# Performance work log

Measured on AMD Instinct MI355X. Metric: run time of the kernel, lower is better.

The kernel has to match this reference:

```python
import jax, jax.numpy as jnp
import numpy as np
from jax import lax

GAT_SLOPE = 0.2   # leaky relu slope inside GATv2 attention
MLP_SLOPE = 0.01  # default nn.LeakyReLU slope in the MLP


def setup_inputs() -> dict:
    key = jax.random.key(0)
    ks = iter(jax.random.split(key, 48))
    nm, nd, C, H = 1500, 800, 128, 8
    E, P = 80000, 40000

    def nrm(shape, s=0.1):
        return jax.random.normal(next(ks), shape, jnp.float32) * s

    inp = {
        "mic_feature": nrm((nm, nm), 1.0),
        "dis_feature": nrm((nd, nd), 1.0),
        "edge_index": jax.random.randint(next(ks), (2, E), 0, nm + nd),
        "pos_pairs": jnp.stack([jax.random.randint(next(ks), (P,), 0, nm),
                                 jax.random.randint(next(ks), (P,), 0, nd)], axis=1),
        "neg_pairs": jnp.stack([jax.random.randint(next(ks), (P,), 0, nm),
                                 jax.random.randint(next(ks), (P,), 0, nd)], axis=1),
        "train_model": 1,
        # projection params
        "W_mic": nrm((nm, C)),
        "W_dis": nrm((nd, C)),
        # GATv2Conv params (lin_l, lin_r, att, out bias); concat=True -> out dim H*C
        "gat_Wl": nrm((C, H * C)),
        "gat_bl": jnp.zeros((H * C,), jnp.float32),
        "gat_Wr": nrm((C, H * C)),
        "gat_br": jnp.zeros((H * C,), jnp.float32),
        "gat_att": nrm((H, C)),
        "gat_bias": jnp.zeros((H * C,), jnp.float32),
        # CNN kernels (heads, k) for k in {1,4,16,32}, 6 out channels
        "cw1": nrm((6, 1, H, 1)),  "cb1": jnp.zeros((6,), jnp.float32),
        "cw4": nrm((6, 1, H, 4)),  "cb4": jnp.zeros((6,), jnp.float32),
        "cw16": nrm((6, 1, H, 16)), "cb16": jnp.zeros((6,), jnp.float32),
        "cw32": nrm((6, 1, H, 32)), "cb32": jnp.zeros((6,), jnp.float32),
        # MLP: 2778 -> 1389 -> 694 -> 463 -> 1 (no bias on last)
        "mw1": nrm((2778, 1389), 0.02), "mb1": jnp.zeros((1389,), jnp.float32),
        "mw2": nrm((1389, 694), 0.02),  "mb2": jnp.zeros((694,), jnp.float32),
        "mw3": nrm((694, 463), 0.02),   "mb3": jnp.zeros((463,), jnp.float32),
        "mw4": nrm((463, 1), 0.05),
    }
    return inp


def _lrelu(x, s):
    return jnp.where(x > 0, x, s * x)


def reference(mic_feature, dis_feature, edge_index, pos_pairs, neg_pairs, train_model,
              W_mic, W_dis, gat_Wl, gat_bl, gat_Wr, gat_br, gat_att, gat_bias,
              cw1, cb1, cw4, cb4, cw16, cb16, cw32, cb32,
              mw1, mb1, mw2, mb2, mw3, mb3, mw4):
    H = gat_att.shape[0]
    # project both node types to common dim and stack: [N, C]
    h = jnp.concatenate([mic_feature @ W_mic, dis_feature @ W_dis], axis=0)
    N, C = h.shape
    # GATv2: separate source/target transforms -> [N, H, C]
    xl = (h @ gat_Wl + gat_bl).reshape(N, H, C)
    xr = (h @ gat_Wr + gat_br).reshape(N, H, C)
    # add self loops (PyG default)
    src = jnp.concatenate([edge_index[0], jnp.arange(N)])
    dst = jnp.concatenate([edge_index[1], jnp.arange(N)])
    z = _lrelu(xl[src] + xr[dst], GAT_SLOPE)           # [E, H, C]
    e = jnp.einsum('ehc,hc->eh', z, gat_att)           # [E, H]
    # segment softmax over incoming edges per destination node
    emax = jax.ops.segment_max(e, dst, num_segments=N)
    ex = jnp.exp(e - emax[dst])
    den = jax.ops.segment_sum(ex, dst, num_segments=N)
    alpha = ex / den[dst]                              # [E, H]
    out = jax.ops.segment_sum(alpha[:, :, None] * xl[src], dst, num_segments=N)
    res = out.reshape(N, H * C) + gat_bias             # [N, H*C]
    # multi-kernel CNN over [N, 1, H, C]
    x4 = res.reshape(N, 1, H, C)

    def conv(w, b):
        y = lax.conv_general_dilated(x4, w, (1, 1), 'VALID',
                                     dimension_numbers=('NCHW', 'OIHW', 'NCHW'))
        return jax.nn.relu(y + b[None, :, None, None]).reshape(N, -1)

    cnn_outputs = jnp.concatenate([conv(cw1, cb1), conv(cw4, cb4),
                                   conv(cw16, cb16), conv(cw32, cb32)], axis=1)
    # vectorized positive/negative pair gather-multiply (replaces python loop)
    nm = mic_feature.shape[0]
    emb_m = cnn_outputs[:nm]
    emb_d = cnn_outputs[nm:]
    pairs = jnp.concatenate([pos_pairs, neg_pairs], axis=0)
    feats = emb_m[pairs[:, 0]] * emb_d[pairs[:, 1]]    # [2P, F]
    labels = jnp.concatenate([jnp.ones((pos_pairs.shape[0], 1), jnp.float32),
                              jnp.zeros((neg_pairs.shape[0], 1), jnp.float32)], axis=0)
    # MLP prediction head (dropout identity at eval)
    hh = _lrelu(feats @ mw1 + mb1, MLP_SLOPE)
    hh = _lrelu(hh @ mw2 + mb2, MLP_SLOPE)
    hh = _lrelu(hh @ mw3 + mb3, MLP_SLOPE)
    pred = jax.nn.sigmoid(hh @ mw4)                    # [2P, 1]
    return (pred, labels, cnn_outputs)
```

## Files before the change

kernel.cpp:

```cpp
#include <hip/hip_runtime.h>


typedef unsigned short u16;
typedef __attribute__((ext_vector_type(8))) short bf16x8;
typedef __attribute__((ext_vector_type(4))) float f32x4;

__device__ __forceinline__ float b2f(u16 u) {
  unsigned v = ((unsigned)u) << 16;
  return __builtin_bit_cast(float, v);
}
__device__ __forceinline__ u16 f2b(float f) {
  unsigned x = __builtin_bit_cast(unsigned, f);
  x += 0x7fffu + ((x >> 16) & 1u);
  return (u16)(x >> 16);
}

__device__ __forceinline__ void async_ld16(const u16* g, u16* l) {
  __builtin_amdgcn_global_load_lds(
      (const __attribute__((address_space(1))) void*)g,
      (__attribute__((address_space(3))) void*)l, 16, 0, 0);
}

__device__ __forceinline__ int sniff_bf16(const void* p, int n) {
  const u16* pu = (const u16*)p;
  int ns = n < 128 ? n : 128;
  int sane = 0, nz = 0;
  for (int i = 0; i < ns; i++) {
    u16 v = pu[i];
    if (v) nz++;
    int e = (v >> 7) & 0xFF;
    if (e >= 100 && e <= 140) sane++;
  }
  return (nz == 0) || (sane * 8 >= ns * 7);
}
__device__ __forceinline__ float ld_any(const void* p, size_t i, int isbf) {
  return isbf ? b2f(((const u16*)p)[i]) : ((const float*)p)[i];
}

__global__ void cvt_f(const void* __restrict__ in, float* __restrict__ out,
                      int n) {
  __shared__ int sbf;
  if (threadIdx.x == 0) sbf = sniff_bf16(in, n);
  __syncthreads();
  int tid = blockIdx.x * 256 + threadIdx.x;
  if (tid < n) out[tid] = ld_any(in, tid, sbf);
}
__global__ void cvt_f_t(const void* __restrict__ in, float* __restrict__ out,
                        int K, int N) {
  __shared__ int sbf;
  if (threadIdx.x == 0) sbf = sniff_bf16(in, K * N);
  __syncthreads();
  int tid = blockIdx.x * 256 + threadIdx.x;
  if (tid >= K * N) return;
  int nn = tid / K, k = tid - nn * K;
  out[tid] = ld_any(in, (size_t)k * N + nn, sbf);
}
__global__ void cvt_b(const void* __restrict__ in, u16* __restrict__ out,
                      int n) {
  __shared__ int sbf;
  if (threadIdx.x == 0) sbf = sniff_bf16(in, n);
  __syncthreads();
  int tid = blockIdx.x * 256 + threadIdx.x;
  if (tid < n) out[tid] = f2b(ld_any(in, tid, sbf));
}
__global__ void cvt_b_tt(const void* __restrict__ in, u16* __restrict__ out,
                         int K, int N, int Kpad, int Npad) {
  __shared__ int sbf;
  __shared__ float tile[32][33];
  if (threadIdx.x == 0) sbf = sniff_bf16(in, K * N);
  __syncthreads();
  int k0 = blockIdx.x * 32, n0 = blockIdx.y * 32;
  int tx = threadIdx.x & 31, ty = threadIdx.x >> 5;
#pragma unroll
  for (int i = 0; i < 32; i += 8) {
    int k = k0 + ty + i, n = n0 + tx;
    tile[ty + i][tx] =
        (k < K && n < N) ? ld_any(in, (size_t)k * N + n, sbf) : 0.f;
  }
  __syncthreads();
#pragma unroll
  for (int i = 0; i < 32; i += 8) {
    int n = n0 + ty + i, k = k0 + tx;
    if (n < Npad && k < Kpad) out[(size_t)n * Kpad + k] = f2b(tile[tx][ty + i]);
  }
}

__global__ void k_feats(const u16* __restrict__ emb,
                        const int* __restrict__ posp,
                        const int* __restrict__ negp, int npos, int mbase,
                        int rows, u16* __restrict__ feats) {
  int idx = blockIdx.x * 256 + threadIdx.x;
  int r = idx / 352, c8 = (idx - r * 352) * 8;
  if (r >= rows) return;
  if (c8 >= 2784) {
    bf16x8 z = {0, 0, 0, 0, 0, 0, 0, 0};
    *(bf16x8*)(feats + (size_t)r * 2816 + c8) = z;
    return;
  }
  int g = mbase + r;
  const int* pp = (g < npos) ? (posp + 2 * g) : (negp + 2 * (g - npos));
  bf16x8 x = *(const bf16x8*)(emb + (size_t)pp[0] * 2784 + c8);
  bf16x8 y = *(const bf16x8*)(emb + (size_t)(1500 + pp[1]) * 2784 + c8);
  bf16x8 v;
#pragma unroll
  for (int j = 0; j < 8; j++)
    ((u16*)&v)[j] = f2b(b2f((u16)x[j]) * b2f((u16)y[j]));
  *(bf16x8*)(feats + (size_t)r * 2816 + c8) = v;
}

__global__ __launch_bounds__(512, 2) void mgemm256(
    const u16* __restrict__ A, const u16* __restrict__ BT,
    const u16* __restrict__ bias, u16* __restrict__ C, int M, int N, int Kpad,
    int lda, int ldb, int ldc, float slope) {
  __shared__ u16 lds[65536];
  u16* As = lds;
  u16* Bs = lds + 32768;
  const int t = threadIdx.x;
  const int lane = t & 63, wave = t >> 6;
  const int quad = lane >> 4, l16 = lane & 15;
  const int wm = wave >> 2, wn = wave & 3;
  const int m0 = blockIdx.y * 256, n0 = blockIdx.x * 256;

  const int r0 = t >> 2;
  const int csrc = (t & 3) ^ ((t >> 3) & 3);
  const u16* Ap = A + (size_t)(m0 + r0) * lda + csrc * 8;
  const u16* Bp = BT + (size_t)(n0 + r0) * ldb + csrc * 8;
  const size_t a128 = (size_t)128 * lda, b128 = (size_t)128 * ldb;
  const int dst = wave * 512;

  const int rsw = (quad ^ ((l16 >> 1) & 3)) * 8;
  const int a_base = (wm * 128 + l16) * 32 + rsw;
  const int b_base = (wn * 64 + l16) * 32 + rsw;

  f32x4 zero4 = {0.f, 0.f, 0.f, 0.f};
  f32x4 acc[8][4];
#pragma unroll
  for (int i = 0; i < 8; i++)
#pragma unroll
    for (int j = 0; j < 4; j++) acc[i][j] = zero4;

  const int iters = Kpad >> 7;

#define ST_A(slab, kofs)                              \
  {                                                   \
    u16* d_ = As + (slab) * 8192 + dst;               \
    async_ld16(Ap + (kofs), d_);                      \
    async_ld16(Ap + a128 + (kofs), d_ + 4096);        \
  }
#define ST_B(slab, kofs)                              \
  {                                                   \
    u16* d_ = Bs + (slab) * 8192 + dst;               \
    async_ld16(Bp + (kofs), d_);                      \
    async_ld16(Bp + b128 + (kofs), d_ + 4096);        \
  }
#define RD_A(slab, i0)                                                       \
  _Pragma("unroll") for (int i = 0; i < 4; i++) af[i] =                      \
      *(const bf16x8*)(As + (slab) * 8192 + a_base + ((i0) + i) * 512);
#define RD_B(slab)                                                           \
  _Pragma("unroll") for (int j = 0; j < 4; j++) bf[j] =                      \
      *(const bf16x8*)(Bs + (slab) * 8192 + b_base + j * 512);
#define MF16(A0)                                                             \
  __builtin_amdgcn_s_barrier();                                              \
  asm volatile("s_waitcnt lgkmcnt(0)" ::: "memory");                         \
  __builtin_amdgcn_sched_barrier(0);                                         \
  __builtin_amdgcn_s_setprio(1);                                             \
  _Pragma("unroll") for (int i = 0; i < 4; i++)                              \
      _Pragma("unroll") for (int j = 0; j < 4; j++) acc[(A0) + i][j] =       \
          __builtin_amdgcn_mfma_f32_16x16x32_bf16(af[i], bf[j],              \
                                                  acc[(A0) + i][j], 0, 0, 0);\
  __builtin_amdgcn_s_setprio(0);
#define WAIT6 asm volatile("s_waitcnt vmcnt(6)" ::: "memory");

  ST_A(0, 0);  ST_B(0, 0);
  ST_A(1, 32); ST_B(1, 32);
  ST_A(2, 64); ST_B(2, 64);
  asm volatile("s_waitcnt vmcnt(6)" ::: "memory");
  __builtin_amdgcn_s_barrier();

  for (int it = 0; it < iters - 1; ++it) {
    const size_t tb = (size_t)it * 128;
    bf16x8 af[4], bf[4];
    RD_A(0, 0); RD_B(0); ST_A(3, tb + 96);          MF16(0);
    RD_A(0, 4);          ST_B(3, tb + 96);  WAIT6;  MF16(4);
    RD_A(1, 0); RD_B(1); ST_A(0, tb + 128);         MF16(0);
    RD_A(1, 4);          ST_B(0, tb + 128); WAIT6;  MF16(4);
    RD_A(2, 0); RD_B(2); ST_A(1, tb + 160);         MF16(0);
    RD_A(2, 4);          ST_B(1, tb + 160); WAIT6;  MF16(4);
    RD_A(3, 0); RD_B(3); ST_A(2, tb + 192);         MF16(0);
    RD_A(3, 4);          ST_B(2, tb + 192); WAIT6;  MF16(4);
  }

  {
    const size_t tb = (size_t)(iters - 1) * 128;
    bf16x8 af[4], bf[4];
    RD_A(0, 0); RD_B(0); ST_A(3, tb + 96);          MF16(0);
    RD_A(0, 4);          ST_B(3, tb + 96);
    asm volatile("s_waitcnt vmcnt(8)" ::: "memory");
    MF16(4);
    RD_A(1, 0); RD_B(1);                            MF16(0);
    RD_A(1, 4);
    asm volatile("s_waitcnt vmcnt(4)" ::: "memory");
    MF16(4);
    RD_A(2, 0); RD_B(2);                            MF16(0);
    RD_A(2, 4);
    asm volatile("s_waitcnt vmcnt(0)" ::: "memory");
    MF16(4);
    RD_A(3, 0); RD_B(3);                            MF16(0);
    RD_A(3, 4);                                     MF16(4);
  }
#undef ST_A
#undef ST_B
#undef RD_A
#undef RD_B
#undef MF16
#undef WAIT6

#pragma unroll
  for (int j = 0; j < 4; j++) {
    int col = n0 + wn * 64 + j * 16 + l16;
    if (col >= ldc) continue;
    float bv = 0.f;
    if (bias != nullptr && col < N) bv = b2f(bias[col]);
#pragma unroll
    for (int i = 0; i < 8; i++) {
#pragma unroll
      for (int r = 0; r < 4; r++) {
        int row = m0 + wm * 128 + i * 16 + quad * 4 + r;
        if (row >= M) continue;
        float v;
        if (col < N) {
          v = acc[i][j][r] + bv;
          v = (v > 0.f) ? v : v * slope;
        } else {
          v = 0.f;
        }
        C[(size_t)row * ldc + col] = f2b(v);
      }
    }
  }
}

__global__ __launch_bounds__(256) void vgemm_f(
    const float* __restrict__ A, const float* __restrict__ BT,
    const float* __restrict__ bias, float* __restrict__ C, int M, int N, int K,
    int lda, int ldb, int ldc) {
  __shared__ float As[16 * 66];
  __shared__ float Bs[64 * 66];
  const int t = threadIdx.x;
  const int m0 = blockIdx.y * 16, n0 = blockIdx.x * 64;
  const int tx = t & 63, ty = t >> 6;
  float acc[4] = {0.f, 0.f, 0.f, 0.f};
  for (int k0 = 0; k0 < K; k0 += 64) {
    for (int idx = t; idx < 16 * 64; idx += 256) {
      int r = idx >> 6, k = idx & 63;
      int m = m0 + r, kk = k0 + k;
      As[r * 66 + k] = (m < M && kk < K) ? A[(size_t)m * lda + kk] : 0.f;
    }
    for (int idx = t; idx < 64 * 64; idx += 256) {
      int nr = idx >> 6, k = idx & 63;
      int nn = n0 + nr, kk = k0 + k;
      Bs[nr * 66 + k] = (nn < N && kk < K) ? BT[(size_t)nn * ldb + kk] : 0.f;
    }
    __syncthreads();
#pragma unroll 8
    for (int k = 0; k < 64; k++) {
      float b = Bs[tx * 66 + k];
#pragma unroll
      for (int q = 0; q < 4; q++) acc[q] += As[(ty * 4 + q) * 66 + k] * b;
    }
    __syncthreads();
  }
  int col = n0 + tx;
  if (col >= N) return;
  float bv = (bias != nullptr) ? bias[col] : 0.f;
#pragma unroll
  for (int q = 0; q < 4; q++) {
    int row = m0 + ty * 4 + q;
    if (row < M) C[(size_t)row * ldc + col] = acc[q] + bv;
  }
}

__global__ __launch_bounds__(256) void vgemm_ks(
    const float* __restrict__ A, const float* __restrict__ BT,
    float* __restrict__ C, int M, int N, int K, int lda, int ldb, int ldc,
    int kchunk) {
  __shared__ float As[16 * 66];
  __shared__ float Bs[64 * 66];
  const int t = threadIdx.x;
  const int m0 = blockIdx.y * 16, n0 = blockIdx.x * 64;
  const int kbeg = blockIdx.z * kchunk;
  int kend = kbeg + kchunk;
  if (kend > K) kend = K;
  const int tx = t & 63, ty = t >> 6;
  float acc[4] = {0.f, 0.f, 0.f, 0.f};
  for (int k0 = kbeg; k0 < kend; k0 += 64) {
    for (int idx = t; idx < 16 * 64; idx += 256) {
      int r = idx >> 6, k = idx & 63;
      int m = m0 + r, kk = k0 + k;
      As[r * 66 + k] = (m < M && kk < kend) ? A[(size_t)m * lda + kk] : 0.f;
    }
    for (int idx = t; idx < 64 * 64; idx += 256) {
      int nr = idx >> 6, k = idx & 63;
      int nn = n0 + nr, kk = k0 + k;
      Bs[nr * 66 + k] = (nn < N && kk < kend) ? BT[(size_t)nn * ldb + kk] : 0.f;
    }
    __syncthreads();
#pragma unroll 8
    for (int k = 0; k < 64; k++) {
      float b = Bs[tx * 66 + k];
#pragma unroll
      for (int q = 0; q < 4; q++) acc[q] += As[(ty * 4 + q) * 66 + k] * b;
    }
    __syncthreads();
  }
  int col = n0 + tx;
  if (col >= N) return;
#pragma unroll
  for (int q = 0; q < 4; q++) {
    int row = m0 + ty * 4 + q;
    if (row < M) atomicAdd(&C[(size_t)row * ldc + col], acc[q]);
  }
}

__global__ void k_zero2(int* __restrict__ a, int* __restrict__ b, int n) {
  int tid = blockIdx.x * 256 + threadIdx.x;
  if (tid < n) { a[tid] = 0; b[tid] = 0; }
}

__global__ void k_zerof(float* __restrict__ a, int n) {
  int tid = blockIdx.x * 256 + threadIdx.x;
  if (tid < n) a[tid] = 0.f;
}

__global__ void k_edge_e(const float* __restrict__ xl,
                         const float* __restrict__ xr,
                         const int* __restrict__ ei,
                         const float* __restrict__ att, float* __restrict__ e,
                         int E, int Etot) {
  __shared__ float attf[1024];
  int t = threadIdx.x;
  for (int i = t; i < 1024; i += 256) attf[i] = att[i];
  __syncthreads();
  int lane = t & 63;
  int eid = blockIdx.x * 4 + (t >> 6);
  if (eid >= Etot) return;
  int src = (eid < E) ? ei[eid] : (eid - E);
  int dst = (eid < E) ? ei[E + eid] : (eid - E);
  const float* pl = xl + (size_t)src * 1024;
  const float* pr = xr + (size_t)dst * 1024;
#pragma unroll
  for (int h = 0; h < 8; h++) {
    float a0 = pl[h * 128 + lane] + pr[h * 128 + lane];
    float a1 = pl[h * 128 + 64 + lane] + pr[h * 128 + 64 + lane];
    a0 = (a0 > 0.f) ? a0 : 0.2f * a0;
    a1 = (a1 > 0.f) ? a1 : 0.2f * a1;
    float p = a0 * attf[h * 128 + lane] + a1 * attf[h * 128 + 64 + lane];
#pragma unroll
    for (int off = 32; off; off >>= 1) p += __shfl_xor(p, off);
    if (lane == 0) e[(size_t)eid * 8 + h] = p;
  }
}

__global__ void k_count(const int* __restrict__ ei, int* __restrict__ cnt,
                        int E, int Etot) {
  int tid = blockIdx.x * 256 + threadIdx.x;
  if (tid >= Etot) return;
  int dst = (tid < E) ? ei[E + tid] : (tid - E);
  atomicAdd(&cnt[dst], 1);
}

__global__ void k_scan(const int* __restrict__ cnt, int* __restrict__ rowstart,
                       int Nn) {
  __shared__ int part[257];
  int t = threadIdx.x;
  int chunk = (Nn + 255) / 256;
  int b = t * chunk;
  int en = b + chunk; if (en > Nn) en = Nn;
  int s = 0;
  for (int i = b; i < en; i++) s += cnt[i];
  part[t] = s;
  __syncthreads();
  if (t == 0) {
    int acc = 0;
    for (int i = 0; i < 256; i++) { int v = part[i]; part[i] = acc; acc += v; }
    part[256] = acc;
  }
  __syncthreads();
  int run = part[t];
  for (int i = b; i < en; i++) { rowstart[i] = run; run += cnt[i]; }
  if (t == 0) rowstart[Nn] = part[256];
}

__global__ void k_scatter(const int* __restrict__ ei,
                          const int* __restrict__ rowstart,
                          int* __restrict__ cur, int* __restrict__ csr, int E,
                          int Etot) {
  int tid = blockIdx.x * 256 + threadIdx.x;
  if (tid >= Etot) return;
  int dst = (tid < E) ? ei[E + tid] : (tid - E);
  int p = atomicAdd(&cur[dst], 1);
  unsigned idx = (unsigned)(rowstart[dst] + p);
  if (idx < (unsigned)Etot) csr[idx] = tid;
}

__global__ void k_softmax(const float* __restrict__ e,
                          const int* __restrict__ csr,
                          const int* __restrict__ rowstart,
                          float* __restrict__ wgt, int Nn, int Etot) {
  int t = threadIdx.x;
  int lane = t & 63;
  int d = blockIdx.x * 4 + (t >> 6);
  if (d >= Nn) return;
  int rs = rowstart[d], re = rowstart[d + 1];
  for (int h = 0; h < 8; h++) {
    float mx = -3.0e38f;
    for (int i = rs + lane; i < re; i += 64) {
      unsigned eid = (unsigned)csr[i];
      if (eid < (unsigned)Etot) mx = fmaxf(mx, e[(size_t)eid * 8 + h]);
    }
#pragma unroll
    for (int off = 32; off; off >>= 1) mx = fmaxf(mx, __shfl_xor(mx, off));
    if (mx < -1.0e37f) mx = 0.f;
    float s = 0.f;
    for (int i = rs + lane; i < re; i += 64) {
      unsigned eid = (unsigned)csr[i];
      if (eid < (unsigned)Etot) s += expf(e[(size_t)eid * 8 + h] - mx);
    }
#pragma unroll
    for (int off = 32; off; off >>= 1) s += __shfl_xor(s, off);
    float inv = (s > 0.f) ? 1.f / s : 0.f;
    for (int i = rs + lane; i < re; i += 64) {
      unsigned eid = (unsigned)csr[i];
      if (eid < (unsigned)Etot)
        wgt[(size_t)eid * 8 + h] = expf(e[(size_t)eid * 8 + h] - mx) * inv;
    }
  }
}

__global__ void k_aggregate(const float* __restrict__ wgt,
                            const float* __restrict__ xl,
                            const int* __restrict__ ei,
                            const int* __restrict__ csr,
                            const int* __restrict__ rowstart,
                            const float* __restrict__ gbias,
                            float* __restrict__ res, int E, int Etot) {
  int d = blockIdx.x;
  int t = threadIdx.x;
  int c = t & 127, hb = t >> 7;
  int rs = rowstart[d], re = rowstart[d + 1];
  float acc[4] = {0.f, 0.f, 0.f, 0.f};
  for (int i = rs; i < re; i++) {
    unsigned eid = (unsigned)csr[i];
    if (eid >= (unsigned)Etot) continue;
    int src = (eid < (unsigned)E) ? ei[eid] : (int)(eid - E);
    const float* px = xl + (size_t)src * 1024 + hb * 512 + c;
    const float* pw = wgt + (size_t)eid * 8 + hb * 4;
#pragma unroll
    for (int q = 0; q < 4; q++) acc[q] += pw[q] * px[q * 128];
  }
#pragma unroll
  for (int q = 0; q < 4; q++) {
    int idx = (hb * 4 + q) * 128 + c;
    res[(size_t)d * 1024 + idx] = acc[q] + gbias[idx];
  }
}

__global__ void k_cnn(const float* __restrict__ res,
                      const float* __restrict__ cw1, const float* __restrict__ cb1,
                      const float* __restrict__ cw4, const float* __restrict__ cb4,
                      const float* __restrict__ cw16, const float* __restrict__ cb16,
                      const float* __restrict__ cw32, const float* __restrict__ cb32,
                      float* __restrict__ outc, u16* __restrict__ emb) {
  __shared__ float xs[1024];
  __shared__ float wc[2544];
  __shared__ float cb[24];
  int t = threadIdx.x, node = blockIdx.x;
  for (int i = t; i < 1024; i += 256) xs[i] = res[(size_t)node * 1024 + i];
  for (int i = t; i < 48; i += 256) wc[i] = cw1[i];
  for (int i = t; i < 192; i += 256) wc[48 + i] = cw4[i];
  for (int i = t; i < 768; i += 256) wc[240 + i] = cw16[i];
  for (int i = t; i < 1536; i += 256) wc[1008 + i] = cw32[i];
  if (t < 6) {
    cb[t] = cb1[t];
    cb[6 + t] = cb4[t];
    cb[12 + t] = cb16[t];
    cb[18 + t] = cb32[t];
  }
  __syncthreads();
  for (int o = t; o < 2778; o += 256) {
    int k, W, base, boff, rr;
    if (o < 768)       { k = 1;  W = 128; base = 0;    boff = 0;  rr = o; }
    else if (o < 1518) { k = 4;  W = 125; base = 48;   boff = 6;  rr = o - 768; }
    else if (o < 2196) { k = 16; W = 113; base = 240;  boff = 12; rr = o - 1518; }
    else               { k = 32; W = 97;  base = 1008; boff = 18; rr = o - 2196; }
    int oc = rr / W, wp = rr - oc * W;
    const float* wgt = &wc[base + oc * 8 * k];
    float v = cb[boff + oc];
    for (int h = 0; h < 8; h++)
      for (int j = 0; j < k; j++) v += xs[h * 128 + wp + j] * wgt[h * k + j];
    v = fmaxf(v, 0.f);
    outc[(size_t)node * 2778 + o] = v;
    emb[(size_t)node * 2784 + o] = f2b(v);
  }
  if (t < 6) emb[(size_t)node * 2784 + 2778 + t] = 0;
}

__global__ void k_gemv_sig(const u16* __restrict__ hh3,
                           const u16* __restrict__ w4, float* __restrict__ pred,
                           int M, int K, int ldk) {
  __shared__ float ws[464];
  int t = threadIdx.x;
  for (int i = t; i < K; i += 256) ws[i] = b2f(w4[i]);
  __syncthreads();
  int lane = t & 63;
  int m = blockIdx.x * 4 + (t >> 6);
  if (m >= M) return;
  const u16* p = hh3 + (size_t)m * ldk;
  float s = 0.f;
  for (int i = lane; i < K; i += 64) s += b2f(p[i]) * ws[i];
#pragma unroll
  for (int off = 32; off; off >>= 1) s += __shfl_xor(s, off);
  if (!(s == s)) s = 0.f;
  s = fminf(fmaxf(s, -30.f), 30.f);
  if (lane == 0) pred[m] = 1.f / (1.f + expf(-s));
}

__global__ void k_labels(float* __restrict__ lab, int P) {
  int tid = blockIdx.x * 256 + threadIdx.x;
  if (tid < 2 * P) lab[tid] = (tid < P) ? 1.f : 0.f;
}

__global__ void k_sentinel(float* __restrict__ pred, int M, float val) {
  int tid = blockIdx.x * 256 + threadIdx.x;
  if (tid < M) pred[tid] = val;
}

extern "C" void kernel_launch(void* const* d_in, const int* in_sizes, int n_in,
                              void* d_out, int out_size, void* d_ws,
                              size_t ws_size, hipStream_t stream) {
  (void)in_sizes; (void)n_in; (void)out_size;
  const int* ei = (const int*)d_in[2];
  const int* posp = (const int*)d_in[3];
  const int* negp = (const int*)d_in[4];

  const int E = 80000, ET = 82300, P = 40000, M = 80000;

  float* outp = (float*)d_out;
  float* outl = outp + 80000;
  float* outc = outp + 160000;

  k_labels<<<(2 * P + 255) / 256, 256, 0, stream>>>(outl, P);

  char* base = (char*)d_ws;
  size_t off = 0;
  auto alloc = [&](size_t bytes) -> void* {
    void* p = base + off;
    off = (off + bytes + 255) & ~(size_t)255;
    return p;
  };
  float* mic_f = (float*)alloc((size_t)1500 * 1500 * 4);
  float* dis_f = (float*)alloc((size_t)800 * 800 * 4);
  float* WmT_f = (float*)alloc((size_t)128 * 1500 * 4);
  float* WdT_f = (float*)alloc((size_t)128 * 800 * 4);
  float* WlT_f = (float*)alloc((size_t)1024 * 128 * 4);
  float* WrT_f = (float*)alloc((size_t)1024 * 128 * 4);
  float* bl_f = (float*)alloc(1024 * 4);
  float* br_f = (float*)alloc(1024 * 4);
  float* att_f = (float*)alloc(1024 * 4);
  float* gbias_f = (float*)alloc(1024 * 4);
  float* cw1_f = (float*)alloc(48 * 4);
  float* cb1_f = (float*)alloc(6 * 4);
  float* cw4_f = (float*)alloc(192 * 4);
  float* cb4_f = (float*)alloc(6 * 4);
  float* cw16_f = (float*)alloc(768 * 4);
  float* cb16_f = (float*)alloc(6 * 4);
  float* cw32_f = (float*)alloc(1536 * 4);
  float* cb32_f = (float*)alloc(6 * 4);
  u16* m1T = (u16*)alloc((size_t)1536 * 2816 * 2);
  u16* m2T = (u16*)alloc((size_t)768 * 1408 * 2);
  u16* m3T = (u16*)alloc((size_t)512 * 768 * 2);
  u16* mb1_b = (u16*)alloc(1389 * 2);
  u16* mb2_b = (u16*)alloc(694 * 2);
  u16* mb3_b = (u16*)alloc(463 * 2);
  u16* mw4_b = (u16*)alloc(463 * 2);
  float* hbuf = (float*)alloc((size_t)2300 * 128 * 4);
  float* xlf = (float*)alloc((size_t)2300 * 1024 * 4);
  float* xrf = (float*)alloc((size_t)2300 * 1024 * 4);
  float* resf = xrf;
  float* ebuf = (float*)alloc((size_t)ET * 8 * 4);
  float* wbuf = (float*)alloc((size_t)ET * 8 * 4);
  u16* emb = (u16*)alloc((size_t)2300 * 2784 * 2);
  int* cnt = (int*)alloc(2300 * 4);
  int* rowst = (int*)alloc(2304 * 4);
  int* cur = (int*)alloc(2300 * 4);
  int* csr = (int*)alloc((size_t)ET * 4);
  size_t fixed_end = off;

  const size_t per_row = (size_t)(2816 + 1408 + 768) * 2;
  size_t avail = (ws_size > fixed_end) ? (ws_size - fixed_end) : 0;
  long long Rll = (long long)(avail / per_row);
  int R = (Rll > M) ? M : (int)Rll;
  R &= ~255;
  if (R > 21760) R = 21760;
  if (fixed_end > ws_size || R < 256) {
    k_sentinel<<<(M + 255) / 256, 256, 0, stream>>>(outp, M, 0.25f);
    return;
  }
  u16* feats = (u16*)(base + fixed_end);
  u16* hh1 = feats + (size_t)R * 2816;
  u16* hh2 = hh1 + (size_t)R * 1408;

  k_zero2<<<(2300 + 255) / 256, 256, 0, stream>>>(cnt, cur, 2300);
  k_zerof<<<(2300 * 128 + 255) / 256, 256, 0, stream>>>(hbuf, 2300 * 128);

  cvt_f<<<(2250000 + 255) / 256, 256, 0, stream>>>(d_in[0], mic_f, 2250000);
  cvt_f<<<(640000 + 255) / 256, 256, 0, stream>>>(d_in[1], dis_f, 640000);
  cvt_f_t<<<(192000 + 255) / 256, 256, 0, stream>>>(d_in[6], WmT_f, 1500, 128);
  cvt_f_t<<<(102400 + 255) / 256, 256, 0, stream>>>(d_in[7], WdT_f, 800, 128);
  cvt_f_t<<<(131072 + 255) / 256, 256, 0, stream>>>(d_in[8], WlT_f, 128, 1024);
  cvt_f<<<4, 256, 0, stream>>>(d_in[9], bl_f, 1024);
  cvt_f_t<<<(131072 + 255) / 256, 256, 0, stream>>>(d_in[10], WrT_f, 128, 1024);
  cvt_f<<<4, 256, 0, stream>>>(d_in[11], br_f, 1024);
  cvt_f<<<4, 256, 0, stream>>>(d_in[12], att_f, 1024);
  cvt_f<<<4, 256, 0, stream>>>(d_in[13], gbias_f, 1024);
  cvt_f<<<1, 256, 0, stream>>>(d_in[14], cw1_f, 48);
  cvt_f<<<1, 256, 0, stream>>>(d_in[15], cb1_f, 6);
  cvt_f<<<1, 256, 0, stream>>>(d_in[16], cw4_f, 192);
  cvt_f<<<1, 256, 0, stream>>>(d_in[17], cb4_f, 6);
  cvt_f<<<3, 256, 0, stream>>>(d_in[18], cw16_f, 768);
  cvt_f<<<1, 256, 0, stream>>>(d_in[19], cb16_f, 6);
  cvt_f<<<6, 256, 0, stream>>>(d_in[20], cw32_f, 1536);
  cvt_f<<<1, 256, 0, stream>>>(d_in[21], cb32_f, 6);
  cvt_b_tt<<<dim3(88, 48), 256, 0, stream>>>(d_in[22], m1T, 2778, 1389, 2816,
                                             1536);
  cvt_b<<<(1389 + 255) / 256, 256, 0, stream>>>(d_in[23], mb1_b, 1389);
  cvt_b_tt<<<dim3(44, 24), 256, 0, stream>>>(d_in[24], m2T, 1389, 694, 1408,
                                             768);
  cvt_b<<<(694 + 255) / 256, 256, 0, stream>>>(d_in[25], mb2_b, 694);
  cvt_b_tt<<<dim3(24, 16), 256, 0, stream>>>(d_in[26], m3T, 694, 463, 768, 512);
  cvt_b<<<(463 + 255) / 256, 256, 0, stream>>>(d_in[27], mb3_b, 463);
  cvt_b<<<(463 + 255) / 256, 256, 0, stream>>>(d_in[28], mw4_b, 463);

  vgemm_ks<<<dim3(2, 94, 8), 256, 0, stream>>>(mic_f, WmT_f, hbuf, 1500, 128,
                                               1500, 1500, 1500, 128, 192);
  vgemm_ks<<<dim3(2, 50, 5), 256, 0, stream>>>(dis_f, WdT_f,
                                               hbuf + (size_t)1500 * 128, 800,
                                               128, 800, 800, 800, 128, 192);
  vgemm_f<<<dim3(16, 144), 256, 0, stream>>>(hbuf, WlT_f, bl_f, xlf, 2300,
                                             1024, 128, 128, 128, 1024);
  vgemm_f<<<dim3(16, 144), 256, 0, stream>>>(hbuf, WrT_f, br_f, xrf, 2300,
                                             1024, 128, 128, 128, 1024);

  k_edge_e<<<(ET + 3) / 4, 256, 0, stream>>>(xlf, xrf, ei, att_f, ebuf, E, ET);
  k_count<<<(ET + 255) / 256, 256, 0, stream>>>(ei, cnt, E, ET);
  k_scan<<<1, 256, 0, stream>>>(cnt, rowst, 2300);
  k_scatter<<<(ET + 255) / 256, 256, 0, stream>>>(ei, rowst, cur, csr, E, ET);
  k_softmax<<<(2300 + 3) / 4, 256, 0, stream>>>(ebuf, csr, rowst, wbuf, 2300, ET);
  k_aggregate<<<2300, 256, 0, stream>>>(wbuf, xlf, ei, csr, rowst, gbias_f,
                                        resf, E, ET);

  k_cnn<<<2300, 256, 0, stream>>>(resf, cw1_f, cb1_f, cw4_f, cb4_f, cw16_f,
                                  cb16_f, cw32_f, cb32_f, outc, emb);

  for (int c0 = 0; c0 < M; c0 += R) {
    int rows = (M - c0 < R) ? (M - c0) : R;
    int gby = (rows + 255) / 256;
    k_feats<<<((size_t)rows * 352 + 255) / 256, 256, 0, stream>>>(
        emb, posp, negp, P, c0, rows, feats);
    mgemm256<<<dim3(6, gby), 512, 0, stream>>>(feats, m1T, mb1_b, hh1, rows,
                                               1389, 2816, 2816, 2816, 1408,
                                               0.01f);
    mgemm256<<<dim3(3, gby), 512, 0, stream>>>(hh1, m2T, mb2_b, hh2, rows, 694,
                                               1408, 1408, 1408, 768, 0.01f);
    mgemm256<<<dim3(2, gby), 512, 0, stream>>>(hh2, m3T, mb3_b, hh1, rows, 463,
                                               768, 768, 768, 480, 0.01f);
    k_gemv_sig<<<(rows + 3) / 4, 256, 0, stream>>>(hh1, mw4_b, outp + c0, rows,
                                                   463, 480);
  }
}
```

Measured before the change: 1.999 ms.

## Double-buffer LDS fragment registers to overlap LDS reads with MFMA

Splits the A/B fragment registers into two sets so that the LDS reads for the next MFMA group are issued before the current MFMA group runs. This replaces the per-step lgkmcnt(0) wait with software pipelining. The aim is to hide LDS read latency behind matrix-core work in the main GEMM loop. In exchange it doubles fragment register usage, which may raise VGPR pressure and reduce occupancy, and it reorders barriers relative to the async global-to-LDS stores.

```diff
diff --git a/kernel.cpp b/kernel.cpp
--- a/kernel.cpp
+++ b/kernel.cpp
@@ -141,6 +141,8 @@
 
   const int iters = Kpad >> 7;
 
+  bf16x8 ra0[4], ra1[4], rb0[4], rb1[4];
+
 #define ST_A(slab, kofs)                              \
   {                                                   \
     u16* d_ = As + (slab) * 8192 + dst;               \
@@ -153,20 +155,19 @@
     async_ld16(Bp + (kofs), d_);                      \
     async_ld16(Bp + b128 + (kofs), d_ + 4096);        \
   }
-#define RD_A(slab, i0)                                                       \
-  _Pragma("unroll") for (int i = 0; i < 4; i++) af[i] =                      \
+#define LDA4(rr, slab, i0)                                                   \
+  _Pragma("unroll") for (int i = 0; i < 4; i++) rr[i] =                      \
       *(const bf16x8*)(As + (slab) * 8192 + a_base + ((i0) + i) * 512);
-#define RD_B(slab)                                                           \
-  _Pragma("unroll") for (int j = 0; j < 4; j++) bf[j] =                      \
+#define LDB4(rr, slab)                                                       \
+  _Pragma("unroll") for (int j = 0; j < 4; j++) rr[j] =                      \
       *(const bf16x8*)(Bs + (slab) * 8192 + b_base + j * 512);
-#define MF16(A0)                                                             \
-  __builtin_amdgcn_s_barrier();                                              \
-  asm volatile("s_waitcnt lgkmcnt(0)" ::: "memory");                         \
-  __builtin_amdgcn_sched_barrier(0);                                         \
+#define BAR __builtin_amdgcn_s_barrier();
+#define SBAR __builtin_amdgcn_sched_barrier(0);
+#define MFMA16(AS, BS, A0)                                                   \
   __builtin_amdgcn_s_setprio(1);                                             \
   _Pragma("unroll") for (int i = 0; i < 4; i++)                              \
       _Pragma("unroll") for (int j = 0; j < 4; j++) acc[(A0) + i][j] =       \
-          __builtin_amdgcn_mfma_f32_16x16x32_bf16(af[i], bf[j],              \
+          __builtin_amdgcn_mfma_f32_16x16x32_bf16(AS[i], BS[j],              \
                                                   acc[(A0) + i][j], 0, 0, 0);\
   __builtin_amdgcn_s_setprio(0);
 #define WAIT6 asm volatile("s_waitcnt vmcnt(6)" ::: "memory");
@@ -175,44 +176,45 @@
   ST_A(1, 32); ST_B(1, 32);
   ST_A(2, 64); ST_B(2, 64);
   asm volatile("s_waitcnt vmcnt(6)" ::: "memory");
-  __builtin_amdgcn_s_barrier();
+  BAR;
+  LDA4(ra0, 0, 0); LDB4(rb0, 0);
 
   for (int it = 0; it < iters - 1; ++it) {
     const size_t tb = (size_t)it * 128;
-    bf16x8 af[4], bf[4];
-    RD_A(0, 0); RD_B(0); ST_A(3, tb + 96);          MF16(0);
-    RD_A(0, 4);          ST_B(3, tb + 96);  WAIT6;  MF16(4);
-    RD_A(1, 0); RD_B(1); ST_A(0, tb + 128);         MF16(0);
-    RD_A(1, 4);          ST_B(0, tb + 128); WAIT6;  MF16(4);
-    RD_A(2, 0); RD_B(2); ST_A(1, tb + 160);         MF16(0);
-    RD_A(2, 4);          ST_B(1, tb + 160); WAIT6;  MF16(4);
-    RD_A(3, 0); RD_B(3); ST_A(2, tb + 192);         MF16(0);
-    RD_A(3, 4);          ST_B(2, tb + 192); WAIT6;  MF16(4);
+    BAR; ST_A(3, tb + 96);          LDA4(ra1, 0, 4);               SBAR; MFMA16(ra0, rb0, 0);
+    BAR; ST_B(3, tb + 96);  WAIT6;  LDA4(ra0, 1, 0); LDB4(rb1, 1); SBAR; MFMA16(ra1, rb0, 4);
+    BAR; ST_A(0, tb + 128);         LDA4(ra1, 1, 4);               SBAR; MFMA16(ra0, rb1, 0);
+    BAR; ST_B(0, tb + 128); WAIT6;  LDA4(ra0, 2, 0); LDB4(rb0, 2); SBAR; MFMA16(ra1, rb1, 4);
+    BAR; ST_A(1, tb + 160);         LDA4(ra1, 2, 4);               SBAR; MFMA16(ra0, rb0, 0);
+    BAR; ST_B(1, tb + 160); WAIT6;  LDA4(ra0, 3, 0); LDB4(rb1, 3); SBAR; MFMA16(ra1, rb0, 4);
+    BAR; ST_A(2, tb + 192);         LDA4(ra1, 3, 4);               SBAR; MFMA16(ra0, rb1, 0);
+    BAR; ST_B(2, tb + 192); WAIT6;  LDA4(ra0, 0, 0); LDB4(rb0, 0); SBAR; MFMA16(ra1, rb1, 4);
   }
 
   {
     const size_t tb = (size_t)(iters - 1) * 128;
-    bf16x8 af[4], bf[4];
-    RD_A(0, 0); RD_B(0); ST_A(3, tb + 96);          MF16(0);
-    RD_A(0, 4);          ST_B(3, tb + 96);
+    BAR; ST_A(3, tb + 96);          LDA4(ra1, 0, 4);               SBAR; MFMA16(ra0, rb0, 0);
+    BAR; ST_B(3, tb + 96);
     asm volatile("s_waitcnt vmcnt(8)" ::: "memory");
-    MF16(4);
-    RD_A(1, 0); RD_B(1);                            MF16(0);
-    RD_A(1, 4);
+    LDA4(ra0, 1, 0); LDB4(rb1, 1);                                 SBAR; MFMA16(ra1, rb0, 4);
+    BAR;                            LDA4(ra1, 1, 4);               SBAR; MFMA16(ra0, rb1, 0);
+    BAR;
     asm volatile("s_waitcnt vmcnt(4)" ::: "memory");
-    MF16(4);
-    RD_A(2, 0); RD_B(2);                            MF16(0);
-    RD_A(2, 4);
+    LDA4(ra0, 2, 0); LDB4(rb0, 2);                                 SBAR; MFMA16(ra1, rb1, 4);
+    BAR;                            LDA4(ra1, 2, 4);               SBAR; MFMA16(ra0, rb0, 0);
+    BAR;
     asm volatile("s_waitcnt vmcnt(0)" ::: "memory");
-    MF16(4);
-    RD_A(3, 0); RD_B(3);                            MF16(0);
-    RD_A(3, 4);                                     MF16(4);
+    LDA4(ra0, 3, 0); LDB4(rb1, 3);                                 SBAR; MFMA16(ra1, rb0, 4);
+    BAR;                            LDA4(ra1, 3, 4);               SBAR; MFMA16(ra0, rb1, 0);
+    BAR;                                                           SBAR; MFMA16(ra1, rb1, 4);
   }
 #undef ST_A
 #undef ST_B
-#undef RD_A
-#undef RD_B
-#undef MF16
+#undef LDA4
+#undef LDB4
+#undef BAR
+#undef SBAR
+#undef MFMA16
 #undef WAIT6
 
 #pragma unroll
```

After: 1.989 ms. Within noise of the previous version (-0.5%).
